# Performance work log

Hardware: AMD Instinct MI355X
Metric: run time of the kernel (lower is better)

The kernel has to match this reference:

```python
import jax, jax.numpy as jnp
import numpy as np
import math

B, N, M, C, H = 4, 2048, 2048, 512, 4
D_V = C // H          # 128, used for scale and value head dim
D_QK = 2 * C // H     # 256, q/k head dim due to seq-axis split of the 2*dim qkv output
SCALE = D_V ** -0.5
EPS = 1e-12           # F.normalize eps


def _l2norm(t):
    n = jnp.linalg.norm(t, axis=-1, keepdims=True)
    return t / jnp.maximum(n, EPS)


def setup_inputs() -> dict:
    key = jax.random.key(0)
    k1, k2, k3, k4 = jax.random.split(key, 4)
    x = jax.random.normal(k1, (B, N, C), dtype=jnp.float32)
    context = jax.random.normal(k2, (B, M, C), dtype=jnp.float32)
    W_qkv = jax.random.normal(k3, (2 * C, C), dtype=jnp.float32) * 0.02  # torch Linear weight [out,in]
    W_proj = jax.random.normal(k4, (C, C), dtype=jnp.float32) * 0.02
    radius = jnp.ones((H,), dtype=jnp.float32) * math.sqrt(D_V)
    return {"x": x, "context": context, "W_qkv": W_qkv, "W_proj": W_proj, "radius": radius}


def reference(x, context, W_qkv, W_proj, radius):
    # qkv(cat([x, context], dim=1)) then split along sequence: q from x rows, k from context rows
    q = jnp.einsum('bnc,oc->bno', x, W_qkv)        # [B,N,2C]
    k = jnp.einsum('bmc,oc->bmo', context, W_qkv)  # [B,M,2C]
    q = q.reshape(B, N, H, D_QK).transpose(0, 2, 1, 3)       # [B,H,N,256]
    k = k.reshape(B, M, H, D_QK).transpose(0, 2, 1, 3)       # [B,H,M,256]
    v = context.reshape(B, M, H, D_V).transpose(0, 2, 1, 3)  # [B,H,M,128]
    r = radius[None, :, None, None]
    q = _l2norm(q) * r
    k = _l2norm(k) * r
    attn = jnp.einsum('bhnd,bhmd->bhnm', q, k) * SCALE
    attn = jax.nn.softmax(attn, axis=-1)
    out = jnp.einsum('bhnm,bhmd->bhnd', attn, v)
    out = out.transpose(0, 2, 1, 3).reshape(B, N, C)
    return jnp.einsum('bnc,oc->bno', out, W_proj)
```

## Files before the change

### kernel.cpp

```cpp
#include <hip/hip_runtime.h>
#include <hip/hip_bf16.h>
#include <stdint.h>

#define SCALE_F 0.08838834764831845f

typedef __attribute__((ext_vector_type(8))) short short8;
typedef __attribute__((ext_vector_type(4))) float f32x4;
typedef __attribute__((ext_vector_type(16))) float f32x16;

__device__ __forceinline__ void g2l16(const void* g, void* l) {
  __builtin_amdgcn_global_load_lds(
      (const __attribute__((address_space(1))) void*)g,
      (__attribute__((address_space(3))) void*)l, 16, 0, 0);
}

__device__ __forceinline__ float bf2f(unsigned short s) {
  union { unsigned int i; float f; } c; c.i = ((unsigned int)s) << 16; return c.f;
}

__global__ __launch_bounds__(256) void convert_xw(
    const float* __restrict__ x, const float* __restrict__ wqkv,
    const float* __restrict__ wproj, __hip_bfloat16* __restrict__ ab,
    __hip_bfloat16* __restrict__ wb, __hip_bfloat16* __restrict__ wpb)
{
  size_t qi = (size_t)blockIdx.x * 256 + threadIdx.x;
  const float* src; __hip_bfloat16* dst; size_t off;
  if (qi < 1048576)      { src = x;     dst = ab;  off = qi; }
  else if (qi < 1179648) { src = wqkv;  dst = wb;  off = qi - 1048576; }
  else                   { src = wproj; dst = wpb; off = qi - 1179648; }
  float4 v = ((const float4*)src)[off];
  union { __hip_bfloat16 h4[4]; uint2 u; } o;
  o.h4[0] = __float2bfloat16(v.x); o.h4[1] = __float2bfloat16(v.y);
  o.h4[2] = __float2bfloat16(v.z); o.h4[3] = __float2bfloat16(v.w);
  ((uint2*)dst)[off] = o.u;
}

__global__ __launch_bounds__(256) void ctx_pack(
    const float* __restrict__ ctx, __hip_bfloat16* __restrict__ vt,
    __hip_bfloat16* __restrict__ ab)
{
  __shared__ float tile[128][33];
  const int bid = blockIdx.x;
  const int mt = bid & 63;
  const int bh = bid >> 6;
  const int h = bh & 3, b = bh >> 2;
  const int tid = threadIdx.x;
  for (int i = 0; i < 16; ++i) {
    int idx = i * 256 + tid;
    int mm = idx >> 7, d = idx & 127;
    size_t gidx = ((size_t)b * 2048 + mt * 32 + mm) * 512 + h * 128 + d;
    float v = ctx[gidx];
    tile[d][mm] = v;
    ab[4194304 + gidx] = __float2bfloat16(v);
  }
  __syncthreads();
  for (int i = 0; i < 16; ++i) {
    int idx = i * 256 + tid;
    int d = idx >> 5, mm = idx & 31;
    vt[((size_t)bh * 128 + d) * 2048 + mt * 32 + mm] = __float2bfloat16(tile[d][mm]);
  }
}

template <typename OUT>
__global__ __launch_bounds__(256) void gemm_nt(
    const __hip_bfloat16* __restrict__ A, const __hip_bfloat16* __restrict__ B,
    OUT* __restrict__ C, int O, int K, int tiles_o)
{
  __shared__ __hip_bfloat16 sA[128 * 32];
  __shared__ __hip_bfloat16 sB[128 * 32];
  const int tid = threadIdx.x;
  const int wave = tid >> 6, lane = tid & 63;
  const int ln = lane & 15, q = lane >> 4;
  const int br = (blockIdx.x / tiles_o) * 128;
  const int bo = (blockIdx.x % tiles_o) * 128;
  const int wr = (wave >> 1) * 64, wc = (wave & 1) * 64;
  const __hip_bfloat16* Ab = A + (size_t)br * K;
  const __hip_bfloat16* Bb = B + (size_t)bo * K;
  const int row0 = tid >> 2, p0 = tid & 3;
  f32x4 acc[4][4] = {};
  for (int k0 = 0; k0 < K; k0 += 32) {
    for (int i = 0; i < 2; ++i) {
      int row = i * 64 + row0;
      g2l16(Ab + (size_t)row * K + k0 + p0 * 8, (char*)sA + (i * 256 + tid) * 16);
      g2l16(Bb + (size_t)row * K + k0 + p0 * 8, (char*)sB + (i * 256 + tid) * 16);
    }
    __syncthreads();
    short8 af[4], bfr[4];
    for (int mi = 0; mi < 4; ++mi)
      af[mi] = *(const short8*)(sA + (wr + mi * 16 + ln) * 32 + q * 8);
    for (int ni = 0; ni < 4; ++ni)
      bfr[ni] = *(const short8*)(sB + (wc + ni * 16 + ln) * 32 + q * 8);
    for (int mi = 0; mi < 4; ++mi)
      for (int ni = 0; ni < 4; ++ni)
        acc[mi][ni] = __builtin_amdgcn_mfma_f32_16x16x32_bf16(af[mi], bfr[ni], acc[mi][ni], 0, 0, 0);
    __syncthreads();
  }
  for (int mi = 0; mi < 4; ++mi)
    for (int ni = 0; ni < 4; ++ni) {
      int rg = br + wr + mi * 16 + q * 4;
      int cg = bo + wc + ni * 16 + ln;
      for (int r = 0; r < 4; ++r) {
        float v = acc[mi][ni][r];
        if constexpr (sizeof(OUT) == 2)
          C[(size_t)(rg + r) * O + cg] = __float2bfloat16(v);
        else
          C[(size_t)(rg + r) * O + cg] = v;
      }
    }
}

__global__ __launch_bounds__(256) void normalize_qk(
    const __hip_bfloat16* __restrict__ proj, const float* __restrict__ radius,
    __hip_bfloat16* __restrict__ qn, __hip_bfloat16* __restrict__ kn)
{
  const int r = blockIdx.x;
  const int h = threadIdx.x >> 6, lane = threadIdx.x & 63;
  union { uint2 u; unsigned short s[4]; } pu;
  pu.u = *(const uint2*)(proj + (size_t)r * 1024 + h * 256 + lane * 4);
  float v0 = bf2f(pu.s[0]), v1 = bf2f(pu.s[1]), v2 = bf2f(pu.s[2]), v3 = bf2f(pu.s[3]);
  float ss = v0 * v0 + v1 * v1 + v2 * v2 + v3 * v3;
  for (int off = 1; off < 64; off <<= 1) ss += __shfl_xor(ss, off);
  float nrm = fmaxf(sqrtf(ss), 1e-12f);
  const bool isq = r < 8192;
  const int rr = isq ? r : r - 8192;
  const float rad = radius[h];
  const float sc = (isq ? rad * rad * SCALE_F : 1.0f) / nrm;
  __hip_bfloat16* dst = (isq ? qn : kn) +
      ((size_t)((rr >> 11) * 4 + h) * 2048 + (rr & 2047)) * 256 + lane * 4;
  union { __hip_bfloat16 h4[4]; uint2 u; } o;
  o.h4[0] = __float2bfloat16(v0 * sc);
  o.h4[1] = __float2bfloat16(v1 * sc);
  o.h4[2] = __float2bfloat16(v2 * sc);
  o.h4[3] = __float2bfloat16(v3 * sc);
  *(uint2*)dst = o.u;
}

__global__ __launch_bounds__(256, 2) void attn(
    const __hip_bfloat16* __restrict__ qn,
    const __hip_bfloat16* __restrict__ kn,
    const __hip_bfloat16* __restrict__ vt,
    float* __restrict__ Op,
    float* __restrict__ den)
{
  __shared__ __hip_bfloat16 sK[3][32 * 256];
  __shared__ __hip_bfloat16 sV[2][128 * 32];
  __shared__ __hip_bfloat16 sP[4][32 * 40];
  const int tid = threadIdx.x, wave = tid >> 6, lane = tid & 63;
  const int m32 = lane & 31, hi = lane >> 5;
  const int i = blockIdx.x;
  const int bh = (i & 7) + 8 * ((i >> 3) & 1);
  const int half = (i >> 4) & 1;
  const int nt = i >> 5;
  const int mbase = half * 1024;
  const __hip_bfloat16* Kp = kn + (size_t)bh * 2048 * 256;
  const __hip_bfloat16* Vp = vt + (size_t)bh * 128 * 2048;

  short8 qf[16];
  {
    const __hip_bfloat16* Q = qn + ((size_t)bh * 2048 + nt * 128 + wave * 32) * 256;
    for (int kk = 0; kk < 16; ++kk)
      qf[kk] = *(const short8*)(Q + m32 * 256 + kk * 16 + hi * 8);
  }

  f32x16 oacc[4];
  float denom[16];
  for (int v = 0; v < 4; ++v)
    for (int j = 0; j < 16; ++j) oacc[v][j] = 0.f;
  for (int j = 0; j < 16; ++j) denom[j] = 0.f;
  __hip_bfloat16* sPw = sP[wave];

#define STAGE_K(tile, buf)                                                   \
  for (int t = 0; t < 4; ++t) {                                              \
    int D = t * 256 + tid, row = D >> 5, cc = D & 31;                        \
    g2l16(Kp + (size_t)(mbase + (tile) * 32 + row) * 256 + ((cc ^ (row & 7)) << 3), \
          (char*)sK[buf] + D * 16);                                          \
  }
#define STAGE_V(tile, buf)                                                   \
  for (int t = 0; t < 2; ++t) {                                              \
    int D = t * 256 + tid, rd = D >> 2, cc = D & 3;                          \
    g2l16(Vp + (size_t)rd * 2048 + mbase + (tile) * 32 + ((cc ^ ((rd >> 1) & 3)) << 3), \
          (char*)sV[buf] + D * 16);                                          \
  }

  STAGE_K(0, 0);
  STAGE_V(0, 0);
  __syncthreads();
  STAGE_K(1, 1);
  f32x16 S_cur;
  for (int j = 0; j < 16; ++j) S_cur[j] = 0.f;
  {
    const __hip_bfloat16* sKc = sK[0];
    for (int kk = 0; kk < 16; ++kk) {
      int c = kk * 2 + hi;
      short8 kf = *(const short8*)(sKc + m32 * 256 + ((c ^ (m32 & 7)) << 3));
      S_cur = __builtin_amdgcn_mfma_f32_32x32x16_bf16(qf[kk], kf, S_cur, 0, 0, 0);
    }
  }
  __syncthreads();

  for (int it = 0; it < 32; ++it) {
    if (it + 2 < 32) { STAGE_K(it + 2, (it + 2) % 3); }
    if (it + 1 < 32) { STAGE_V(it + 1, (it + 1) & 1); }
    f32x16 S_next;
    for (int j = 0; j < 16; ++j) S_next[j] = 0.f;
    if (it + 1 < 32) {
      const __hip_bfloat16* sKc = sK[(it + 1) % 3];
      for (int kk = 0; kk < 16; ++kk) {
        int c = kk * 2 + hi;
        short8 kf = *(const short8*)(sKc + m32 * 256 + ((c ^ (m32 & 7)) << 3));
        S_next = __builtin_amdgcn_mfma_f32_32x32x16_bf16(qf[kk], kf, S_next, 0, 0, 0);
      }
    }
    for (int reg = 0; reg < 16; ++reg) {
      float e = __expf(S_cur[reg]);
      denom[reg] += e;
      int row = (reg & 3) + 8 * (reg >> 2) + 4 * hi;
      sPw[row * 40 + m32] = __float2bfloat16(e);
    }
    asm volatile("s_waitcnt lgkmcnt(0)" ::: "memory");
    const __hip_bfloat16* sVc = sV[it & 1];
    for (int kc = 0; kc < 2; ++kc) {
      short8 pf = *(const short8*)(sPw + m32 * 40 + kc * 16 + hi * 8);
      for (int vi = 0; vi < 4; ++vi) {
        int rd = vi * 32 + m32;
        int c = kc * 2 + hi;
        short8 vf = *(const short8*)(sVc + rd * 32 + ((c ^ ((rd >> 1) & 3)) << 3));
        oacc[vi] = __builtin_amdgcn_mfma_f32_32x32x16_bf16(pf, vf, oacc[vi], 0, 0, 0);
      }
    }
    __syncthreads();
    S_cur = S_next;
  }
#undef STAGE_K
#undef STAGE_V

  for (int reg = 0; reg < 16; ++reg)
    for (int off = 1; off < 32; off <<= 1)
      denom[reg] += __shfl_xor(denom[reg], off);

  float* Opb = Op + ((size_t)(half * 16 + bh) * 2048 + nt * 128 + wave * 32) * 128;
  float* denb = den + (size_t)(half * 16 + bh) * 2048 + nt * 128 + wave * 32;
  for (int vi = 0; vi < 4; ++vi)
    for (int reg = 0; reg < 16; ++reg) {
      int row = (reg & 3) + 8 * (reg >> 2) + 4 * hi;
      Opb[(size_t)row * 128 + vi * 32 + m32] = oacc[vi][reg];
    }
  if (m32 == 0)
    for (int reg = 0; reg < 16; ++reg)
      denb[(reg & 3) + 8 * (reg >> 2) + 4 * hi] = denom[reg];
}

__global__ __launch_bounds__(256) void combine(
    const float* __restrict__ Op, const float* __restrict__ den,
    __hip_bfloat16* __restrict__ ob)
{
  int qi = blockIdx.x * 256 + threadIdx.x;
  int r = qi >> 5, dq = qi & 31;
  int bh = r >> 11, n = r & 2047, b = bh >> 2, h = bh & 3;
  float4 o0 = ((const float4*)Op)[qi];
  float4 o1 = ((const float4*)(Op + 4194304))[qi];
  float inv = 1.0f / (den[r] + den[32768 + r]);
  union { __hip_bfloat16 h4[4]; uint2 u; } o;
  o.h4[0] = __float2bfloat16((o0.x + o1.x) * inv);
  o.h4[1] = __float2bfloat16((o0.y + o1.y) * inv);
  o.h4[2] = __float2bfloat16((o0.z + o1.z) * inv);
  o.h4[3] = __float2bfloat16((o0.w + o1.w) * inv);
  *(uint2*)&ob[((size_t)b * 2048 + n) * 512 + h * 128 + dq * 4] = o.u;
}

extern "C" void kernel_launch(void* const* d_in, const int* in_sizes, int n_in,
                              void* d_out, int out_size, void* d_ws, size_t ws_size,
                              hipStream_t stream) {
  const float* x      = (const float*)d_in[0];
  const float* ctx    = (const float*)d_in[1];
  const float* wqkv   = (const float*)d_in[2];
  const float* wproj  = (const float*)d_in[3];
  const float* radius = (const float*)d_in[4];
  char* ws = (char*)d_ws;
  __hip_bfloat16* ab  = (__hip_bfloat16*)(ws);
  __hip_bfloat16* wb  = (__hip_bfloat16*)(ws + 16777216);
  __hip_bfloat16* wpb = (__hip_bfloat16*)(ws + 17825792);
  __hip_bfloat16* proj= (__hip_bfloat16*)(ws + 18350080);
  float*          Op  = (float*)(ws + 18350080);
  float*          den = (float*)(ws + 51904512);
  __hip_bfloat16* qn  = (__hip_bfloat16*)(ws + 85458944);
  __hip_bfloat16* kn  = (__hip_bfloat16*)(ws + 102236160);
  __hip_bfloat16* vt  = (__hip_bfloat16*)(ws + 119013376);
  __hip_bfloat16* ob  = (__hip_bfloat16*)(ws + 127401984);
  float* out = (float*)d_out;

  convert_xw<<<4864, 256, 0, stream>>>(x, wqkv, wproj, ab, wb, wpb);
  ctx_pack<<<1024, 256, 0, stream>>>(ctx, vt, ab);
  gemm_nt<__hip_bfloat16><<<1024, 256, 0, stream>>>(ab, wb, proj, 1024, 512, 8);
  normalize_qk<<<16384, 256, 0, stream>>>(proj, radius, qn, kn);
  attn<<<512, 256, 0, stream>>>(qn, kn, vt, Op, den);
  combine<<<4096, 256, 0, stream>>>(Op, den, ob);
  gemm_nt<float><<<256, 256, 0, stream>>>(ob, wpb, out, 512, 512, 4);
}
```

Measured before the change: 227.5 us.

## Merge prep kernels and alternate QK/PV phase order across co-resident attention blocks

Merges the convert and context-pack kernels into one launch, branching on block index, to save a kernel launch and its gap. In the attention kernel, blocks with odd parity run exp+PV before the next QK MFMA block, while even-parity blocks keep the original order. With two blocks per CU, the two orders are meant to stagger exp/VALU and MFMA work between co-resident blocks so that more of them overlap. Both loop variants are compiled into the kernel, which raises code size. It may also raise register pressure, and the gain depends on which blocks the scheduler actually pairs on a CU.

```diff
diff --git a/kernel.cpp b/kernel.cpp
--- a/kernel.cpp
+++ b/kernel.cpp
@@ -18,46 +18,44 @@
   union { unsigned int i; float f; } c; c.i = ((unsigned int)s) << 16; return c.f;
 }
 
-__global__ __launch_bounds__(256) void convert_xw(
-    const float* __restrict__ x, const float* __restrict__ wqkv,
-    const float* __restrict__ wproj, __hip_bfloat16* __restrict__ ab,
-    __hip_bfloat16* __restrict__ wb, __hip_bfloat16* __restrict__ wpb)
-{
-  size_t qi = (size_t)blockIdx.x * 256 + threadIdx.x;
-  const float* src; __hip_bfloat16* dst; size_t off;
-  if (qi < 1048576)      { src = x;     dst = ab;  off = qi; }
-  else if (qi < 1179648) { src = wqkv;  dst = wb;  off = qi - 1048576; }
-  else                   { src = wproj; dst = wpb; off = qi - 1179648; }
-  float4 v = ((const float4*)src)[off];
-  union { __hip_bfloat16 h4[4]; uint2 u; } o;
-  o.h4[0] = __float2bfloat16(v.x); o.h4[1] = __float2bfloat16(v.y);
-  o.h4[2] = __float2bfloat16(v.z); o.h4[3] = __float2bfloat16(v.w);
-  ((uint2*)dst)[off] = o.u;
-}
-
-__global__ __launch_bounds__(256) void ctx_pack(
-    const float* __restrict__ ctx, __hip_bfloat16* __restrict__ vt,
-    __hip_bfloat16* __restrict__ ab)
-{
-  __shared__ float tile[128][33];
-  const int bid = blockIdx.x;
-  const int mt = bid & 63;
-  const int bh = bid >> 6;
-  const int h = bh & 3, b = bh >> 2;
-  const int tid = threadIdx.x;
-  for (int i = 0; i < 16; ++i) {
-    int idx = i * 256 + tid;
-    int mm = idx >> 7, d = idx & 127;
-    size_t gidx = ((size_t)b * 2048 + mt * 32 + mm) * 512 + h * 128 + d;
-    float v = ctx[gidx];
-    tile[d][mm] = v;
-    ab[4194304 + gidx] = __float2bfloat16(v);
-  }
-  __syncthreads();
-  for (int i = 0; i < 16; ++i) {
-    int idx = i * 256 + tid;
-    int d = idx >> 5, mm = idx & 31;
-    vt[((size_t)bh * 128 + d) * 2048 + mt * 32 + mm] = __float2bfloat16(tile[d][mm]);
+__global__ __launch_bounds__(256) void prep(
+    const float* __restrict__ x, const float* __restrict__ ctx,
+    const float* __restrict__ wqkv, const float* __restrict__ wproj,
+    __hip_bfloat16* __restrict__ ab, __hip_bfloat16* __restrict__ wb,
+    __hip_bfloat16* __restrict__ wpb, __hip_bfloat16* __restrict__ vt)
+{
+  if (blockIdx.x < 4864) {
+    size_t qi = (size_t)blockIdx.x * 256 + threadIdx.x;
+    const float* src; __hip_bfloat16* dst; size_t off;
+    if (qi < 1048576)      { src = x;     dst = ab;  off = qi; }
+    else if (qi < 1179648) { src = wqkv;  dst = wb;  off = qi - 1048576; }
+    else                   { src = wproj; dst = wpb; off = qi - 1179648; }
+    float4 v = ((const float4*)src)[off];
+    union { __hip_bfloat16 h4[4]; uint2 u; } o;
+    o.h4[0] = __float2bfloat16(v.x); o.h4[1] = __float2bfloat16(v.y);
+    o.h4[2] = __float2bfloat16(v.z); o.h4[3] = __float2bfloat16(v.w);
+    ((uint2*)dst)[off] = o.u;
+  } else {
+    __shared__ float tile[128][33];
+    const int bid = blockIdx.x - 4864;
+    const int mt = bid & 63;
+    const int bh = bid >> 6;
+    const int h = bh & 3, b = bh >> 2;
+    const int tid = threadIdx.x;
+    for (int i = 0; i < 16; ++i) {
+      int idx = i * 256 + tid;
+      int mm = idx >> 7, d = idx & 127;
+      size_t gidx = ((size_t)b * 2048 + mt * 32 + mm) * 512 + h * 128 + d;
+      float v = ctx[gidx];
+      tile[d][mm] = v;
+      ab[4194304 + gidx] = __float2bfloat16(v);
+    }
+    __syncthreads();
+    for (int i = 0; i < 16; ++i) {
+      int idx = i * 256 + tid;
+      int d = idx >> 5, mm = idx & 31;
+      vt[((size_t)bh * 128 + d) * 2048 + mt * 32 + mm] = __float2bfloat16(tile[d][mm]);
+    }
   }
 }
 
@@ -152,6 +150,7 @@
   const int half = (i >> 4) & 1;
   const int nt = i >> 5;
   const int mbase = half * 1024;
+  const int parity = (i >> 8) & 1;
   const __hip_bfloat16* Kp = kn + (size_t)bh * 2048 * 256;
   const __hip_bfloat16* Vp = vt + (size_t)bh * 128 * 2048;
 
@@ -181,6 +180,36 @@
     g2l16(Vp + (size_t)rd * 2048 + mbase + (tile) * 32 + ((cc ^ ((rd >> 1) & 3)) << 3), \
           (char*)sV[buf] + D * 16);                                          \
   }
+#define QK_BLOCK(S, buf)                                                     \
+  {                                                                          \
+    const __hip_bfloat16* sKc = sK[buf];                                     \
+    for (int kk = 0; kk < 16; ++kk) {                                        \
+      int c = kk * 2 + hi;                                                   \
+      short8 kf = *(const short8*)(sKc + m32 * 256 + ((c ^ (m32 & 7)) << 3)); \
+      S = __builtin_amdgcn_mfma_f32_32x32x16_bf16(qf[kk], kf, S, 0, 0, 0);   \
+    }                                                                        \
+  }
+#define EXP_BLOCK                                                            \
+  for (int reg = 0; reg < 16; ++reg) {                                       \
+    float e = __expf(S_cur[reg]);                                            \
+    denom[reg] += e;                                                         \
+    int row = (reg & 3) + 8 * (reg >> 2) + 4 * hi;                           \
+    sPw[row * 40 + m32] = __float2bfloat16(e);                               \
+  }
+#define PV_BLOCK(vbuf)                                                       \
+  {                                                                          \
+    asm volatile("s_waitcnt lgkmcnt(0)" ::: "memory");                       \
+    const __hip_bfloat16* sVc = sV[vbuf];                                    \
+    for (int kc = 0; kc < 2; ++kc) {                                         \
+      short8 pf = *(const short8*)(sPw + m32 * 40 + kc * 16 + hi * 8);       \
+      for (int vi = 0; vi < 4; ++vi) {                                       \
+        int rd = vi * 32 + m32;                                              \
+        int c = kc * 2 + hi;                                                 \
+        short8 vf = *(const short8*)(sVc + rd * 32 + ((c ^ ((rd >> 1) & 3)) << 3)); \
+        oacc[vi] = __builtin_amdgcn_mfma_f32_32x32x16_bf16(pf, vf, oacc[vi], 0, 0, 0); \
+      }                                                                      \
+    }                                                                        \
+  }
 
   STAGE_K(0, 0);
   STAGE_V(0, 0);
@@ -188,51 +217,39 @@
   STAGE_K(1, 1);
   f32x16 S_cur;
   for (int j = 0; j < 16; ++j) S_cur[j] = 0.f;
-  {
-    const __hip_bfloat16* sKc = sK[0];
-    for (int kk = 0; kk < 16; ++kk) {
-      int c = kk * 2 + hi;
-      short8 kf = *(const short8*)(sKc + m32 * 256 + ((c ^ (m32 & 7)) << 3));
-      S_cur = __builtin_amdgcn_mfma_f32_32x32x16_bf16(qf[kk], kf, S_cur, 0, 0, 0);
-    }
-  }
+  QK_BLOCK(S_cur, 0);
   __syncthreads();
 
-  for (int it = 0; it < 32; ++it) {
-    if (it + 2 < 32) { STAGE_K(it + 2, (it + 2) % 3); }
-    if (it + 1 < 32) { STAGE_V(it + 1, (it + 1) & 1); }
-    f32x16 S_next;
-    for (int j = 0; j < 16; ++j) S_next[j] = 0.f;
-    if (it + 1 < 32) {
-      const __hip_bfloat16* sKc = sK[(it + 1) % 3];
-      for (int kk = 0; kk < 16; ++kk) {
-        int c = kk * 2 + hi;
-        short8 kf = *(const short8*)(sKc + m32 * 256 + ((c ^ (m32 & 7)) << 3));
-        S_next = __builtin_amdgcn_mfma_f32_32x32x16_bf16(qf[kk], kf, S_next, 0, 0, 0);
-      }
-    }
-    for (int reg = 0; reg < 16; ++reg) {
-      float e = __expf(S_cur[reg]);
-      denom[reg] += e;
-      int row = (reg & 3) + 8 * (reg >> 2) + 4 * hi;
-      sPw[row * 40 + m32] = __float2bfloat16(e);
-    }
-    asm volatile("s_waitcnt lgkmcnt(0)" ::: "memory");
-    const __hip_bfloat16* sVc = sV[it & 1];
-    for (int kc = 0; kc < 2; ++kc) {
-      short8 pf = *(const short8*)(sPw + m32 * 40 + kc * 16 + hi * 8);
-      for (int vi = 0; vi < 4; ++vi) {
-        int rd = vi * 32 + m32;
-        int c = kc * 2 + hi;
-        short8 vf = *(const short8*)(sVc + rd * 32 + ((c ^ ((rd >> 1) & 3)) << 3));
-        oacc[vi] = __builtin_amdgcn_mfma_f32_32x32x16_bf16(pf, vf, oacc[vi], 0, 0, 0);
-      }
-    }
-    __syncthreads();
-    S_cur = S_next;
+  if (parity == 0) {
+    for (int it = 0; it < 32; ++it) {
+      if (it + 2 < 32) { STAGE_K(it + 2, (it + 2) % 3); }
+      if (it + 1 < 32) { STAGE_V(it + 1, (it + 1) & 1); }
+      f32x16 S_next;
+      for (int j = 0; j < 16; ++j) S_next[j] = 0.f;
+      if (it + 1 < 32) QK_BLOCK(S_next, (it + 1) % 3);
+      EXP_BLOCK;
+      PV_BLOCK(it & 1);
+      __syncthreads();
+      S_cur = S_next;
+    }
+  } else {
+    for (int it = 0; it < 32; ++it) {
+      if (it + 2 < 32) { STAGE_K(it + 2, (it + 2) % 3); }
+      if (it + 1 < 32) { STAGE_V(it + 1, (it + 1) & 1); }
+      EXP_BLOCK;
+      PV_BLOCK(it & 1);
+      f32x16 S_next;
+      for (int j = 0; j < 16; ++j) S_next[j] = 0.f;
+      if (it + 1 < 32) QK_BLOCK(S_next, (it + 1) % 3);
+      __syncthreads();
+      S_cur = S_next;
+    }
   }
 #undef STAGE_K
 #undef STAGE_V
+#undef QK_BLOCK
+#undef EXP_BLOCK
+#undef PV_BLOCK
 
   for (int reg = 0; reg < 16; ++reg)
     for (int off = 1; off < 32; off <<= 1)
@@ -289,8 +306,7 @@
   __hip_bfloat16* ob  = (__hip_bfloat16*)(ws + 127401984);
   float* out = (float*)d_out;
 
-  convert_xw<<<4864, 256, 0, stream>>>(x, wqkv, wproj, ab, wb, wpb);
-  ctx_pack<<<1024, 256, 0, stream>>>(ctx, vt, ab);
+  prep<<<5888, 256, 0, stream>>>(x, ctx, wqkv, wproj, ab, wb, wpb, vt);
   gemm_nt<__hip_bfloat16><<<1024, 256, 0, stream>>>(ab, wb, proj, 1024, 512, 8);
   normalize_qk<<<16384, 256, 0, stream>>>(proj, radius, qn, kn);
   attn<<<512, 256, 0, stream>>>(qn, kn, vt, Op, den);
```

Result: no change. 228.2 us (+0.3%).
